# Performance work log

Hardware: AMD Instinct MI355X
Metric: run time of the kernel (lower is better)

The kernel has to match this reference:

```python
import jax, jax.numpy as jnp
import numpy as np

N = 4096
D_MODEL = 512


def setup_inputs() -> dict:
    key = jax.random.key(0)
    ks = jax.random.split(key, 5)
    scale = 1.0 / np.sqrt(D_MODEL)
    return {
        "x": jax.random.normal(ks[0], (N, D_MODEL), dtype=jnp.float32),
        "Wq": jax.random.normal(ks[1], (D_MODEL, D_MODEL), dtype=jnp.float32) * scale,
        "Wk": jax.random.normal(ks[2], (D_MODEL, D_MODEL), dtype=jnp.float32) * scale,
        "Wv": jax.random.normal(ks[3], (D_MODEL, D_MODEL), dtype=jnp.float32) * scale,
        "Ws": jax.random.normal(ks[4], (1, D_MODEL), dtype=jnp.float32) * scale,
    }


def reference(x, Wq, Wk, Wv, Ws):
    # x: [N, d]; torch nn.Linear(bias=False) computes x @ W.T
    Q = x @ Wq.T  # [N, d]
    K = x @ Wk.T  # [N, d]
    V = x @ Wv.T  # [N, d]
    sigma = jnp.clip(x @ Ws.T, 0.001, 1.0)  # [N, 1]

    # prior association: Gaussian kernel over |i - j| with per-row sigma
    pos = jnp.arange(sigma.shape[0], dtype=jnp.float32)
    diff = jnp.abs(pos[:, None] - pos[None, :])  # [N, N]
    gaussian = jnp.exp(-0.5 * (diff / sigma) ** 2) / jnp.sqrt(2.0 * jnp.pi * sigma)
    P = gaussian / (gaussian.sum(axis=1, keepdims=True) + 1e-8)

    scale = jnp.sqrt(jnp.float32(x.shape[-1]))
    S = jax.nn.softmax((Q @ K.T) / scale, axis=-1)  # [N, N]
    Z = S @ V  # [N, d]
    return Z, P, S
```

## Files before the change

kernel.cpp:

```cpp
#include <hip/hip_runtime.h>
#include <math.h>

#define N_TOK 4096
#define DM 512

typedef _Float16 f16x8 __attribute__((ext_vector_type(8)));
typedef _Float16 f16x4 __attribute__((ext_vector_type(4)));
typedef float f32x4 __attribute__((ext_vector_type(4)));

__device__ __forceinline__ void async_ld16(const ushort* g, ushort* l) {
  __builtin_amdgcn_global_load_lds(
      (const __attribute__((address_space(1))) void*)g,
      (__attribute__((address_space(3))) void*)l, 16, 0, 0);
}

template <int N>
__device__ __forceinline__ void vm_wait() {
  asm volatile("s_waitcnt vmcnt(%0)" ::"i"(N) : "memory");
}

__global__ __launch_bounds__(256) void pack_sigma(
    const float* __restrict__ x, const float* __restrict__ Wq,
    const float* __restrict__ Wk, const float* __restrict__ Wv,
    const float* __restrict__ Ws, _Float16* __restrict__ x16,
    _Float16* __restrict__ Wc16, float* __restrict__ sg) {
  const int b = blockIdx.x;
  const int t = threadIdx.x;
  if (b < 2048) {
    int i = b * 1024 + t * 4;
    float4 v = *(const float4*)&x[i];
    f16x4 o;
    o.x = (_Float16)v.x; o.y = (_Float16)v.y;
    o.z = (_Float16)v.z; o.w = (_Float16)v.w;
    *(f16x4*)&x16[i] = o;
    int col = (t * 4) & 511;
    float4 w = *(const float4*)&Ws[col];
    float p = v.x * w.x + v.y * w.y + v.z * w.z + v.w * w.w;
    __shared__ float red[256];
    red[t] = p;
    __syncthreads();
    int lt = t & 127;
    for (int off = 64; off > 0; off >>= 1) {
      if (lt < off) red[t] += red[t + off];
      __syncthreads();
    }
    if (lt == 0) {
      float s = red[t];
      sg[2 * b + (t >> 7)] = fminf(fmaxf(s, 0.001f), 1.0f);
    }
  } else {
    int e = (b - 2048) * 1024 + t * 4;
    const float* src;
    int le = e & (DM * DM - 1);
    if (e < DM * DM) src = Wq + le;
    else if (e < 2 * DM * DM) src = Wk + le;
    else src = Wv + le;
    float4 v = *(const float4*)src;
    f16x4 o;
    o.x = (_Float16)v.x; o.y = (_Float16)v.y;
    o.z = (_Float16)v.z; o.w = (_Float16)v.w;
    *(f16x4*)&Wc16[e] = o;
  }
}

template <int BM, int BN, int BK, int NT, int EPI, int FUSE_P>
__global__ __launch_bounds__(256) void gemm_pipe(
    const _Float16* __restrict__ A, int lda, const _Float16* __restrict__ B,
    int ldb, float scale, float* __restrict__ Cf, _Float16* __restrict__ D0,
    _Float16* __restrict__ D1, _Float16* __restrict__ D2,
    const float* __restrict__ sigma, float* __restrict__ P) {
  constexpr int TB = (BM + BN) * BK;
  constexpr int ACH = BM * BK / 8;
  constexpr int BCH = BN * BK / 8;
  constexpr int L = (ACH + BCH) / 256;
  constexpr int MI = BM / 32;
  constexpr int NJ = BN / 32;
  __shared__ _Float16 lds[3 * TB];
  const int t = threadIdx.x;

  if (FUSE_P && blockIdx.y >= 64) {
    float* red = (float*)lds;
    const int pidx = (blockIdx.y - 64) * 4 + blockIdx.x;
    const int w = t >> 6, lane = t & 63;
#pragma unroll 1
    for (int rr = 0; rr < 4; ++rr) {
      const int i = pidx * 4 + rr;
      const float sgv = sigma[i];
      const float inv2 = -0.5f / (sgv * sgv);
      const float cc = rsqrtf(6.283185307179586f * sgv);
      float4 g[4];
      float sum = 0.f;
#pragma unroll
      for (int r = 0; r < 4; ++r) {
        int j = r * 1024 + t * 4;
        float d0 = (float)(i - j);
        float d1 = d0 - 1.f, d2 = d0 - 2.f, d3 = d0 - 3.f;
        g[r].x = __expf(inv2 * d0 * d0) * cc;
        g[r].y = __expf(inv2 * d1 * d1) * cc;
        g[r].z = __expf(inv2 * d2 * d2) * cc;
        g[r].w = __expf(inv2 * d3 * d3) * cc;
        sum += g[r].x + g[r].y + g[r].z + g[r].w;
      }
#pragma unroll
      for (int off = 32; off > 0; off >>= 1) sum += __shfl_xor(sum, off);
      if (lane == 0) red[w] = sum;
      __syncthreads();
      const float inv = 1.0f / (red[0] + red[1] + red[2] + red[3] + 1e-8f);
      float* Prow = P + (size_t)i * N_TOK;
#pragma unroll
      for (int r = 0; r < 4; ++r) {
        g[r].x *= inv; g[r].y *= inv; g[r].z *= inv; g[r].w *= inv;
        *(float4*)&Prow[r * 1024 + t * 4] = g[r];
      }
      __syncthreads();
    }
    return;
  }

  const int w = t >> 6, Ln = t & 63;
  const int wm = (w >> 1) * (BM / 2), wn = (w & 1) * (BN / 2);
  const int row = Ln & 15, quad = Ln >> 4;

  int bm, bn;
  if constexpr (EPI == 2) {
    const int lb = blockIdx.x + 4 * blockIdx.y;
    const int xcd = lb & 7, idx = lb >> 3;
    bm = ((xcd << 3) | (idx >> 2)) * BM;
    bn = (idx & 3) * BN;
  } else {
    bm = blockIdx.y * BM;
    bn = blockIdx.x * BN;
  }

  f32x4 acc[MI][NJ] = {{}};

  const ushort* gp[L];
#pragma unroll
  for (int k = 0; k < L; ++k) {
    int c = t + k * 256;
    if (c < ACH) {
      int r = c / (BK / 8), c8 = c % (BK / 8);
      gp[k] = (const ushort*)(A + (size_t)(bm + r) * lda + c8 * 8);
    } else {
      int cb = c - ACH;
      int r = cb / (BK / 8), c8 = cb % (BK / 8);
      gp[k] = (const ushort*)(B + (size_t)(bn + r) * ldb + c8 * 8);
    }
  }

  auto stage = [&](int buf) {
    _Float16* dst = lds + buf * TB;
#pragma unroll
    for (int k = 0; k < L; ++k) {
      async_ld16(gp[k], (ushort*)(dst + (t + k * 256) * 8));
      gp[k] += BK;
    }
  };

  stage(0);
  stage(1);

  for (int tt = 0; tt < NT; ++tt) {
    const int cur = tt % 3;
    if (tt + 2 < NT) stage((tt + 2) % 3);
    if (tt < NT - 2) vm_wait<2 * L>();
    else if (tt == NT - 2) vm_wait<L>();
    else vm_wait<0>();
    __builtin_amdgcn_s_barrier();

    const _Float16* Ah = lds + cur * TB;
    const _Float16* Bh = Ah + BM * BK;
    f16x8 af[BK / 32][MI], bf[BK / 32][NJ];
#pragma unroll
    for (int kk = 0; kk < BK / 32; ++kk) {
#pragma unroll
      for (int i = 0; i < MI; ++i)
        af[kk][i] =
            *(const f16x8*)&Ah[(wm + i * 16 + row) * BK + kk * 32 + quad * 8];
#pragma unroll
      for (int j = 0; j < NJ; ++j)
        bf[kk][j] =
            *(const f16x8*)&Bh[(wn + j * 16 + row) * BK + kk * 32 + quad * 8];
    }
#pragma unroll
    for (int kk = 0; kk < BK / 32; ++kk)
#pragma unroll
      for (int i = 0; i < MI; ++i)
#pragma unroll
        for (int j = 0; j < NJ; ++j)
          acc[i][j] = __builtin_amdgcn_mfma_f32_16x16x32_f16(
              af[kk][i], bf[kk][j], acc[i][j], 0, 0, 0);

    asm volatile("s_waitcnt lgkmcnt(0)" ::: "memory");
    __builtin_amdgcn_s_barrier();
  }

  if constexpr (EPI == 1) {
    const int region = bn >> 9;
    _Float16* D = (region == 0) ? D0 : ((region == 1) ? D1 : D2);
#pragma unroll
    for (int i = 0; i < MI; ++i)
#pragma unroll
      for (int j = 0; j < NJ; ++j)
#pragma unroll
        for (int r = 0; r < 4; ++r) {
          int gr = bm + wm + i * 16 + quad * 4 + r;
          int nn = (bn & 511) + wn + j * 16 + row;
          D[(size_t)gr * 512 + nn] = (_Float16)acc[i][j][r];
        }
  } else if constexpr (EPI == 3) {
#pragma unroll
    for (int i = 0; i < MI; ++i)
#pragma unroll
      for (int j = 0; j < NJ; ++j)
#pragma unroll
        for (int r = 0; r < 4; ++r) {
          int gr = bm + wm + i * 16 + quad * 4 + r;
          int gc = bn + wn + j * 16 + row;
          D0[(size_t)gr * N_TOK + gc] = (_Float16)(acc[i][j][r] * scale);
        }
  } else {
#pragma unroll
    for (int i = 0; i < MI; ++i)
#pragma unroll
      for (int j = 0; j < NJ; ++j)
#pragma unroll
        for (int r = 0; r < 4; ++r) {
          int gr = bm + wm + i * 16 + quad * 4 + r;
          int gc = bn + wn + j * 16 + row;
          Cf[(size_t)gr * DM + gc] = acc[i][j][r];
        }
  }
}

__global__ __launch_bounds__(256) void transpose16(
    const _Float16* __restrict__ V16, _Float16* __restrict__ VT) {
  __shared__ _Float16 T[32][34];
  const int t = threadIdx.x;
  const int r = t >> 3, c4 = (t & 7) * 4;
  f16x4 v = *(const f16x4*)&V16[(size_t)(blockIdx.y * 32 + r) * 512 +
                                blockIdx.x * 32 + c4];
  T[r][c4] = v.x; T[r][c4 + 1] = v.y; T[r][c4 + 2] = v.z; T[r][c4 + 3] = v.w;
  __syncthreads();
  f16x4 o;
  o.x = T[c4][r]; o.y = T[c4 + 1][r]; o.z = T[c4 + 2][r]; o.w = T[c4 + 3][r];
  *(f16x4*)&VT[(size_t)(blockIdx.x * 32 + r) * 4096 + blockIdx.y * 32 + c4] = o;
}

__global__ __launch_bounds__(256) void softmax_kernel(
    _Float16* __restrict__ Sc, float* __restrict__ S) {
  __shared__ float red[8];
  const int t = threadIdx.x;
  const int w = t >> 6, lane = t & 63;
  _Float16* Srow16 = Sc + (size_t)blockIdx.x * N_TOK;
  float* Srow = S + (size_t)blockIdx.x * N_TOK;
  float f[16];
  float m = -INFINITY;
#pragma unroll
  for (int r = 0; r < 4; ++r) {
    f16x4 h = *(const f16x4*)&Srow16[r * 1024 + t * 4];
    f[r * 4 + 0] = (float)h.x; f[r * 4 + 1] = (float)h.y;
    f[r * 4 + 2] = (float)h.z; f[r * 4 + 3] = (float)h.w;
    m = fmaxf(m, fmaxf(fmaxf(f[r * 4], f[r * 4 + 1]),
                       fmaxf(f[r * 4 + 2], f[r * 4 + 3])));
  }
#pragma unroll
  for (int off = 32; off > 0; off >>= 1) m = fmaxf(m, __shfl_xor(m, off));
  if (lane == 0) red[w] = m;
  __syncthreads();
  m = fmaxf(fmaxf(red[0], red[1]), fmaxf(red[2], red[3]));
  float sum = 0.f;
#pragma unroll
  for (int i = 0; i < 16; ++i) {
    f[i] = __expf(f[i] - m);
    sum += f[i];
  }
#pragma unroll
  for (int off = 32; off > 0; off >>= 1) sum += __shfl_xor(sum, off);
  if (lane == 0) red[4 + w] = sum;
  __syncthreads();
  const float inv = 1.0f / (red[4] + red[5] + red[6] + red[7]);
#pragma unroll
  for (int r = 0; r < 4; ++r) {
    float4 o;
    o.x = f[r * 4 + 0] * inv; o.y = f[r * 4 + 1] * inv;
    o.z = f[r * 4 + 2] * inv; o.w = f[r * 4 + 3] * inv;
    *(float4*)&Srow[r * 1024 + t * 4] = o;
    f16x4 h;
    h.x = (_Float16)o.x; h.y = (_Float16)o.y;
    h.z = (_Float16)o.z; h.w = (_Float16)o.w;
    *(f16x4*)&Srow16[r * 1024 + t * 4] = h;
  }
}

__global__ __launch_bounds__(256) void tailP(const float* __restrict__ sigma,
                                             float* __restrict__ P) {
  __shared__ float red[256];
  const int t = threadIdx.x;
  const int i = blockIdx.x;
  const float sg = sigma[i];
  const float inv2 = -0.5f / (sg * sg);
  const float c = rsqrtf(6.283185307179586f * sg);
  float4 g[4];
  float sum = 0.f;
#pragma unroll
  for (int r = 0; r < 4; ++r) {
    int j = r * 1024 + t * 4;
    float d0 = (float)(i - j);
    float d1 = d0 - 1.f, d2 = d0 - 2.f, d3 = d0 - 3.f;
    g[r].x = __expf(inv2 * d0 * d0) * c;
    g[r].y = __expf(inv2 * d1 * d1) * c;
    g[r].z = __expf(inv2 * d2 * d2) * c;
    g[r].w = __expf(inv2 * d3 * d3) * c;
    sum += g[r].x + g[r].y + g[r].z + g[r].w;
  }
  red[t] = sum;
  __syncthreads();
  for (int off = 128; off > 0; off >>= 1) {
    if (t < off) red[t] += red[t + off];
    __syncthreads();
  }
  const float inv = 1.0f / (red[0] + 1e-8f);
  float* Prow = P + (size_t)i * N_TOK;
#pragma unroll
  for (int r = 0; r < 4; ++r) {
    g[r].x *= inv; g[r].y *= inv; g[r].z *= inv; g[r].w *= inv;
    *(float4*)&Prow[r * 1024 + t * 4] = g[r];
  }
}

extern "C" void kernel_launch(void* const* d_in, const int* in_sizes, int n_in,
                              void* d_out, int out_size, void* d_ws,
                              size_t ws_size, hipStream_t stream) {
  const float* x = (const float*)d_in[0];
  const float* Wq = (const float*)d_in[1];
  const float* Wk = (const float*)d_in[2];
  const float* Wv = (const float*)d_in[3];
  const float* Ws = (const float*)d_in[4];

  float* out = (float*)d_out;
  float* Z = out;
  float* Pout = Z + (size_t)N_TOK * DM;
  float* S = Pout + (size_t)N_TOK * N_TOK;

  const size_t E = (size_t)N_TOK * DM;

  _Float16* x16 = (_Float16*)d_ws;
  _Float16* Wc16 = x16 + E;
  float* sg = (float*)(Wc16 + 3 * DM * DM);
  _Float16* stage = (_Float16*)(sg + 4096);

  const size_t stage_bytes = (4 * E + (size_t)N_TOK * N_TOK) * sizeof(_Float16);
  const size_t base_bytes = (size_t)((char*)stage - (char*)d_ws);
  const bool ws_ok = ws_size >= base_bytes + stage_bytes;

  _Float16* Q16 = ws_ok ? stage : (_Float16*)Pout;
  _Float16* K16 = Q16 + E;
  _Float16* V16 = K16 + E;
  _Float16* VT16 = V16 + E;
  _Float16* Sc16 = VT16 + E;

  const dim3 blk(256);
  const float qk_scale = 1.0f / sqrtf((float)DM);

  pack_sigma<<<2816, blk, 0, stream>>>(x, Wq, Wk, Wv, Ws, x16, Wc16, sg);

  gemm_pipe<128, 128, 32, 16, 1, 0><<<dim3(12, 32), blk, 0, stream>>>(
      x16, DM, Wc16, DM, 1.0f, nullptr, Q16, K16, V16, nullptr, nullptr);

  transpose16<<<dim3(16, 128), blk, 0, stream>>>(V16, VT16);

  gemm_pipe<256, 128, 32, 16, 3, 0><<<dim3(32, 16), blk, 0, stream>>>(
      Q16, DM, K16, DM, qk_scale, nullptr, Sc16, nullptr, nullptr, nullptr,
      nullptr);

  softmax_kernel<<<N_TOK, blk, 0, stream>>>(Sc16, S);

  if (ws_ok) {
    gemm_pipe<64, 128, 64, 64, 2, 1><<<dim3(4, 64 + 256), blk, 0, stream>>>(
        Sc16, N_TOK, VT16, N_TOK, 1.0f, Z, nullptr, nullptr, nullptr, sg, Pout);
  } else {
    gemm_pipe<64, 128, 64, 64, 2, 0><<<dim3(4, 64), blk, 0, stream>>>(
        Sc16, N_TOK, VT16, N_TOK, 1.0f, Z, nullptr, nullptr, nullptr, nullptr,
        nullptr);
    tailP<<<N_TOK, blk, 0, stream>>>(sg, Pout);
  }
}
```

Before: 245.7 us.

## Fuse V transpose into softmax launch and retile S@V GEMM to 128x128

Folds the V transpose into the softmax kernel as extra blocks, which removes one kernel launch. The S@V GEMM moves from 64x128 tiles with BK=64 to 128x128 tiles with BK=32, and the grid halves to 32 GEMM row blocks plus the P-computation blocks. The P-block start index and the XCD mapping are generalized through a PSTART template parameter. Larger tiles raise per-block reuse but leave fewer GEMM blocks (128) to spread across the CUs, and the two concurrent stages share the same kernel.

After: 260.8 us. +6.1%, slower.

```diff
diff --git a/kernel.cpp b/kernel.cpp
--- a/kernel.cpp
+++ b/kernel.cpp
@@ -63,7 +63,7 @@
   }
 }
 
-template <int BM, int BN, int BK, int NT, int EPI, int FUSE_P>
+template <int BM, int BN, int BK, int NT, int EPI, int PSTART>
 __global__ __launch_bounds__(256) void gemm_pipe(
     const _Float16* __restrict__ A, int lda, const _Float16* __restrict__ B,
     int ldb, float scale, float* __restrict__ Cf, _Float16* __restrict__ D0,
@@ -78,9 +78,9 @@
   __shared__ _Float16 lds[3 * TB];
   const int t = threadIdx.x;
 
-  if (FUSE_P && blockIdx.y >= 64) {
+  if (PSTART && blockIdx.y >= PSTART) {
     float* red = (float*)lds;
-    const int pidx = (blockIdx.y - 64) * 4 + blockIdx.x;
+    const int pidx = (blockIdx.y - PSTART) * 4 + blockIdx.x;
     const int w = t >> 6, lane = t & 63;
 #pragma unroll 1
     for (int rr = 0; rr < 4; ++rr) {
@@ -125,7 +125,7 @@
   if constexpr (EPI == 2) {
     const int lb = blockIdx.x + 4 * blockIdx.y;
     const int xcd = lb & 7, idx = lb >> 3;
-    bm = ((xcd << 3) | (idx >> 2)) * BM;
+    bm = (xcd * (PSTART / 8) + (idx >> 2)) * BM;
     bn = (idx & 3) * BN;
   } else {
     bm = blockIdx.y * BM;
@@ -233,27 +233,28 @@
   }
 }
 
-__global__ __launch_bounds__(256) void transpose16(
+__global__ __launch_bounds__(256) void softmax_vt(
+    _Float16* __restrict__ Sc, float* __restrict__ S,
     const _Float16* __restrict__ V16, _Float16* __restrict__ VT) {
-  __shared__ _Float16 T[32][34];
   const int t = threadIdx.x;
-  const int r = t >> 3, c4 = (t & 7) * 4;
-  f16x4 v = *(const f16x4*)&V16[(size_t)(blockIdx.y * 32 + r) * 512 +
-                                blockIdx.x * 32 + c4];
-  T[r][c4] = v.x; T[r][c4 + 1] = v.y; T[r][c4 + 2] = v.z; T[r][c4 + 3] = v.w;
-  __syncthreads();
-  f16x4 o;
-  o.x = T[c4][r]; o.y = T[c4 + 1][r]; o.z = T[c4 + 2][r]; o.w = T[c4 + 3][r];
-  *(f16x4*)&VT[(size_t)(blockIdx.x * 32 + r) * 4096 + blockIdx.y * 32 + c4] = o;
-}
-
-__global__ __launch_bounds__(256) void softmax_kernel(
-    _Float16* __restrict__ Sc, float* __restrict__ S) {
+  const int b = blockIdx.x;
+  if (b >= N_TOK) {
+    __shared__ _Float16 T[32][34];
+    const int idx = b - N_TOK;
+    const int bx = idx & 15, by = idx >> 4;
+    const int r = t >> 3, c4 = (t & 7) * 4;
+    f16x4 v = *(const f16x4*)&V16[(size_t)(by * 32 + r) * 512 + bx * 32 + c4];
+    T[r][c4] = v.x; T[r][c4 + 1] = v.y; T[r][c4 + 2] = v.z; T[r][c4 + 3] = v.w;
+    __syncthreads();
+    f16x4 o;
+    o.x = T[c4][r]; o.y = T[c4 + 1][r]; o.z = T[c4 + 2][r]; o.w = T[c4 + 3][r];
+    *(f16x4*)&VT[(size_t)(bx * 32 + r) * 4096 + by * 32 + c4] = o;
+    return;
+  }
   __shared__ float red[8];
-  const int t = threadIdx.x;
   const int w = t >> 6, lane = t & 63;
-  _Float16* Srow16 = Sc + (size_t)blockIdx.x * N_TOK;
-  float* Srow = S + (size_t)blockIdx.x * N_TOK;
+  _Float16* Srow16 = Sc + (size_t)b * N_TOK;
+  float* Srow = S + (size_t)b * N_TOK;
   float f[16];
   float m = -INFINITY;
 #pragma unroll
@@ -368,19 +369,17 @@
   gemm_pipe<128, 128, 32, 16, 1, 0><<<dim3(12, 32), blk, 0, stream>>>(
       x16, DM, Wc16, DM, 1.0f, nullptr, Q16, K16, V16, nullptr, nullptr);
 
-  transpose16<<<dim3(16, 128), blk, 0, stream>>>(V16, VT16);
-
   gemm_pipe<256, 128, 32, 16, 3, 0><<<dim3(32, 16), blk, 0, stream>>>(
       Q16, DM, K16, DM, qk_scale, nullptr, Sc16, nullptr, nullptr, nullptr,
       nullptr);
 
-  softmax_kernel<<<N_TOK, blk, 0, stream>>>(Sc16, S);
+  softmax_vt<<<dim3(4096 + 2048), blk, 0, stream>>>(Sc16, S, V16, VT16);
 
   if (ws_ok) {
-    gemm_pipe<64, 128, 64, 64, 2, 1><<<dim3(4, 64 + 256), blk, 0, stream>>>(
+    gemm_pipe<128, 128, 32, 128, 2, 32><<<dim3(4, 32 + 256), blk, 0, stream>>>(
         Sc16, N_TOK, VT16, N_TOK, 1.0f, Z, nullptr, nullptr, nullptr, sg, Pout);
   } else {
-    gemm_pipe<64, 128, 64, 64, 2, 0><<<dim3(4, 64), blk, 0, stream>>>(
+    gemm_pipe<128, 128, 32, 128, 2, 0><<<dim3(4, 32), blk, 0, stream>>>(
         Sc16, N_TOK, VT16, N_TOK, 1.0f, Z, nullptr, nullptr, nullptr, nullptr,
         nullptr);
     tailP<<<N_TOK, blk, 0, stream>>>(sg, Pout);
```
